# Kernel optimization log

Measured on AMD Instinct MI355X. Metric: run time of the kernel, lower is better.

Reference implementation:

```python
import jax, jax.numpy as jnp
import numpy as np

D = 768
LAYERS = 4
LN_EPS = 1e-5


def _layer_norm(h, g, b):
    m = jnp.mean(h, axis=-1, keepdims=True)
    v = jnp.var(h, axis=-1, keepdims=True)
    return (h - m) * jax.lax.rsqrt(v + LN_EPS) * g + b


def _encode(ids, emb, ln_g, ln_b, w1, b1, w2, b2):
    # ids: [N, F] int, emb: [F, V, D] stacked embedding tables
    h = emb[0][ids[:, 0]]
    for i in range(1, emb.shape[0]):
        h = h + emb[i][ids[:, i]]
    h = _layer_norm(h, ln_g, ln_b)
    h = jax.nn.gelu(jnp.dot(h, w1) + b1)
    return jnp.dot(h, w2) + b2


def setup_inputs() -> dict:
    key = jax.random.key(0)
    ks = jax.random.split(key, 24)
    N, E = 50000, 100000
    s = 0.02
    inp = {
        "x": jax.random.randint(ks[0], (N, 9), 0, 128),
        "edge_attr": jax.random.randint(ks[1], (E, 3), 0, 8),
        "edge_index": jax.random.randint(ks[2], (2, E), 0, N),
        # AtomEncoder params
        "atom_emb": jax.random.normal(ks[3], (9, 128, D), jnp.float32) * s,
        "atom_ln_g": jnp.ones((D,), jnp.float32),
        "atom_ln_b": jnp.zeros((D,), jnp.float32),
        "atom_w1": jax.random.normal(ks[4], (D, D), jnp.float32) * s,
        "atom_b1": jnp.zeros((D,), jnp.float32),
        "atom_w2": jax.random.normal(ks[5], (D, D), jnp.float32) * s,
        "atom_b2": jnp.zeros((D,), jnp.float32),
        # BondEncoder params
        "bond_emb": jax.random.normal(ks[6], (3, 8, D), jnp.float32) * s,
        "bond_ln_g": jnp.ones((D,), jnp.float32),
        "bond_ln_b": jnp.zeros((D,), jnp.float32),
        "bond_w1": jax.random.normal(ks[7], (D, D), jnp.float32) * s,
        "bond_b1": jnp.zeros((D,), jnp.float32),
        "bond_w2": jax.random.normal(ks[8], (D, D), jnp.float32) * s,
        "bond_b2": jnp.zeros((D,), jnp.float32),
        # Per-layer GINEConv MLPs + LayerNorms (stacked over layers)
        "conv_w1": jax.random.normal(ks[9], (LAYERS, D, D), jnp.float32) * s,
        "conv_b1": jnp.zeros((LAYERS, D), jnp.float32),
        "conv_w2": jax.random.normal(ks[10], (LAYERS, D, D), jnp.float32) * s,
        "conv_b2": jnp.zeros((LAYERS, D), jnp.float32),
        "ln_g": jnp.ones((LAYERS, D), jnp.float32),
        "ln_b": jnp.zeros((LAYERS, D), jnp.float32),
    }
    return inp


def reference(x, edge_attr, edge_index,
              atom_emb, atom_ln_g, atom_ln_b, atom_w1, atom_b1, atom_w2, atom_b2,
              bond_emb, bond_ln_g, bond_ln_b, bond_w1, bond_b1, bond_w2, bond_b2,
              conv_w1, conv_b1, conv_w2, conv_b2, ln_g, ln_b):
    N = x.shape[0]
    src, dst = edge_index[0], edge_index[1]
    h = _encode(x, atom_emb, atom_ln_g, atom_ln_b, atom_w1, atom_b1, atom_w2, atom_b2)
    e = _encode(edge_attr, bond_emb, bond_ln_g, bond_ln_b, bond_w1, bond_b1, bond_w2, bond_b2)
    for l in range(LAYERS):
        h_in = h
        # GINEConv (eps=0): out = MLP(x + sum_{j in N(i)} relu(x_j + e_ij))
        msg = jax.nn.relu(h[src] + e)                       # [E, D] gather + edge-add + relu
        agg = jax.ops.segment_sum(msg, dst, num_segments=N)  # scatter-add to nodes
        z = h + agg
        z = jnp.dot(jax.nn.relu(jnp.dot(z, conv_w1[l]) + conv_b1[l]), conv_w2[l]) + conv_b2[l]
        # gelu -> dropout (identity at eval) -> residual LayerNorm
        h = _layer_norm(jax.nn.gelu(z) + h_in, ln_g[l], ln_b[l])
    return h
```

## Files before the change

### kernel.cpp

```cpp
#include <hip/hip_runtime.h>


#define DM 768
#define NLAYERS 4
#define CHUNK 50048

typedef _Float16 f16;
typedef __attribute__((ext_vector_type(8))) _Float16 f16x8;
typedef __attribute__((ext_vector_type(4))) _Float16 f16x4;
typedef __attribute__((ext_vector_type(4))) float f32x4;

__device__ __forceinline__ float gelu_f(float x) {
    float u = 0.7978845608028654f * (x + 0.044715f * x * x * x);
    float a = __expf(-2.0f * fabsf(u));
    float t = (1.0f - a) / (1.0f + a);
    t = copysignf(t, u);
    return 0.5f * x * (1.0f + t);
}
__device__ __forceinline__ void async16(const void* g, void* l) {
    __builtin_amdgcn_global_load_lds((const __attribute__((address_space(1))) void*)g,
                                     (__attribute__((address_space(3))) void*)l,
                                     16, 0, 0);
}

__device__ __forceinline__ int xcd_swizzle(int b, int nb) {
    int xcd = b & 7;
    int pos = b >> 3;
    int q = nb >> 3, r = nb & 7;
    int base = (xcd < r) ? xcd * (q + 1) : r * (q + 1) + (xcd - r) * q;
    return base + pos;
}

__global__ __launch_bounds__(256) void transpose768(
    const float* __restrict__ W, f16* __restrict__ Wt) {
    __shared__ float t[32][33];
    int tx = threadIdx.x, ty = threadIdx.y;
    int c0 = blockIdx.x * 32, r0 = blockIdx.y * 32;
    #pragma unroll
    for (int j = 0; j < 32; j += 8) t[ty + j][tx] = W[(r0 + ty + j) * DM + c0 + tx];
    __syncthreads();
    #pragma unroll
    for (int j = 0; j < 32; j += 8) Wt[(long)(c0 + ty + j) * DM + r0 + tx] = (f16)t[tx][ty + j];
}

__global__ __launch_bounds__(256) void embed_ln_wave(
    const int* __restrict__ ids, int F, int V,
    const float* __restrict__ emb,
    const float* __restrict__ g, const float* __restrict__ b,
    f16* __restrict__ out, int M) {
    int row = blockIdx.x * 4 + (threadIdx.x >> 6);
    if (row >= M) return;
    int lane = threadIdx.x & 63;
    int base = lane * 12;

    float v[12];
    #pragma unroll
    for (int j = 0; j < 12; ++j) v[j] = 0.f;
    for (int f = 0; f < F; ++f) {
        int id = ids[(long)row * F + f];
        const float* r = emb + ((long)f * V + id) * DM + base;
        float4 r0 = *(const float4*)&r[0];
        float4 r1 = *(const float4*)&r[4];
        float4 r2 = *(const float4*)&r[8];
        v[0] += r0.x; v[1] += r0.y; v[2]  += r0.z; v[3]  += r0.w;
        v[4] += r1.x; v[5] += r1.y; v[6]  += r1.z; v[7]  += r1.w;
        v[8] += r2.x; v[9] += r2.y; v[10] += r2.z; v[11] += r2.w;
    }
    float s1 = 0.f, s2 = 0.f;
    #pragma unroll
    for (int j = 0; j < 12; ++j) { s1 += v[j]; s2 += v[j] * v[j]; }
    #pragma unroll
    for (int off = 32; off > 0; off >>= 1) {
        s1 += __shfl_xor(s1, off);
        s2 += __shfl_xor(s2, off);
    }
    float mean = s1 * (1.f / DM);
    float var = s2 * (1.f / DM) - mean * mean;
    float rstd = rsqrtf(var + 1e-5f);

    float4 gv0 = *(const float4*)&g[base], gv1 = *(const float4*)&g[base + 4], gv2 = *(const float4*)&g[base + 8];
    float4 bv0 = *(const float4*)&b[base], bv1 = *(const float4*)&b[base + 4], bv2 = *(const float4*)&b[base + 8];
    float gg[12] = {gv0.x, gv0.y, gv0.z, gv0.w, gv1.x, gv1.y, gv1.z, gv1.w, gv2.x, gv2.y, gv2.z, gv2.w};
    float bb[12] = {bv0.x, bv0.y, bv0.z, bv0.w, bv1.x, bv1.y, bv1.z, bv1.w, bv2.x, bv2.y, bv2.z, bv2.w};
    f16* o = out + (long)row * DM + base;
    #pragma unroll
    for (int q = 0; q < 3; ++q) {
        f16x4 ov;
        #pragma unroll
        for (int r = 0; r < 4; ++r)
            ov[r] = (f16)((v[q * 4 + r] - mean) * rstd * gg[q * 4 + r] + bb[q * 4 + r]);
        *(f16x4*)&o[q * 4] = ov;
    }
}

template <typename OUT>
__global__ __launch_bounds__(256) void gelu_res_ln_wave(
    const f16* __restrict__ U, const f16* __restrict__ hin,
    const float* __restrict__ g, const float* __restrict__ b,
    OUT* __restrict__ out, int M) {
    int row = blockIdx.x * 4 + (threadIdx.x >> 6);
    if (row >= M) return;
    int lane = threadIdx.x & 63;
    int base = lane * 12;

    const f16* up = U + (long)row * DM + base;
    const f16* hp = hin + (long)row * DM + base;
    float v[12];
    #pragma unroll
    for (int q = 0; q < 3; ++q) {
        f16x4 uv = *(const f16x4*)&up[q * 4];
        f16x4 hv = *(const f16x4*)&hp[q * 4];
        #pragma unroll
        for (int r = 0; r < 4; ++r)
            v[q * 4 + r] = gelu_f((float)uv[r]) + (float)hv[r];
    }
    float s1 = 0.f, s2 = 0.f;
    #pragma unroll
    for (int j = 0; j < 12; ++j) { s1 += v[j]; s2 += v[j] * v[j]; }
    #pragma unroll
    for (int off = 32; off > 0; off >>= 1) {
        s1 += __shfl_xor(s1, off);
        s2 += __shfl_xor(s2, off);
    }
    float mean = s1 * (1.f / DM);
    float var = s2 * (1.f / DM) - mean * mean;
    float rstd = rsqrtf(var + 1e-5f);

    float4 gv0 = *(const float4*)&g[base], gv1 = *(const float4*)&g[base + 4], gv2 = *(const float4*)&g[base + 8];
    float4 bv0 = *(const float4*)&b[base], bv1 = *(const float4*)&b[base + 4], bv2 = *(const float4*)&b[base + 8];
    float gg[12] = {gv0.x, gv0.y, gv0.z, gv0.w, gv1.x, gv1.y, gv1.z, gv1.w, gv2.x, gv2.y, gv2.z, gv2.w};
    float bb[12] = {bv0.x, bv0.y, bv0.z, bv0.w, bv1.x, bv1.y, bv1.z, bv1.w, bv2.x, bv2.y, bv2.z, bv2.w};
    #pragma unroll
    for (int q = 0; q < 3; ++q) {
        float w0 = (v[q * 4 + 0] - mean) * rstd * gg[q * 4 + 0] + bb[q * 4 + 0];
        float w1 = (v[q * 4 + 1] - mean) * rstd * gg[q * 4 + 1] + bb[q * 4 + 1];
        float w2 = (v[q * 4 + 2] - mean) * rstd * gg[q * 4 + 2] + bb[q * 4 + 2];
        float w3 = (v[q * 4 + 3] - mean) * rstd * gg[q * 4 + 3] + bb[q * 4 + 3];
        if constexpr (sizeof(OUT) == 2) {
            f16x4 ov; ov[0] = (f16)w0; ov[1] = (f16)w1; ov[2] = (f16)w2; ov[3] = (f16)w3;
            *(f16x4*)&out[(long)row * DM + base + q * 4] = ov;
        } else {
            float4 ov; ov.x = w0; ov.y = w1; ov.z = w2; ov.w = w3;
            *(float4*)&out[(long)row * DM + base + q * 4] = ov;
        }
    }
}

__global__ __launch_bounds__(256) void make_combo_ids(
    int V, int nC, int* __restrict__ ids) {
    int c = blockIdx.x * 256 + threadIdx.x;
    if (c >= nC) return;
    ids[c * 3 + 0] = c / (V * V);
    ids[c * 3 + 1] = (c / V) % V;
    ids[c * 3 + 2] = c % V;
}
__global__ __launch_bounds__(256) void make_key_kernel(
    const int* __restrict__ ea, int E, int V, int* __restrict__ key) {
    int e = blockIdx.x * 256 + threadIdx.x;
    if (e >= E) return;
    key[e] = (ea[e * 3 + 0] * V + ea[e * 3 + 1]) * V + ea[e * 3 + 2];
}

__global__ __launch_bounds__(256) void build_list_kernel(
    const int* __restrict__ ei, int E,
    int* __restrict__ head, int* __restrict__ nxt) {
    int e = blockIdx.x * 256 + threadIdx.x;
    if (e >= E) return;
    int dst = ei[E + e];
    nxt[e] = atomicExch(&head[dst], e);
}

__global__ __launch_bounds__(256) void gather_agg_kernel(
    const int* __restrict__ ei,
    const int* __restrict__ head, const int* __restrict__ nxt,
    const int* __restrict__ key,
    const f16* __restrict__ h, const f16* __restrict__ T,
    f16* __restrict__ z, int N) {
    int node = blockIdx.x * 4 + (threadIdx.x >> 6);
    if (node >= N) return;
    int lane = threadIdx.x & 63;
    int base = lane * 12;

    const f16* hr = h + (long)node * DM + base;
    f16x4 v0 = *(const f16x4*)&hr[0];
    f16x4 v1 = *(const f16x4*)&hr[4];
    f16x4 v2 = *(const f16x4*)&hr[8];
    float acc[12];
    #pragma unroll
    for (int j = 0; j < 4; ++j) {
        acc[j]     = (float)v0[j];
        acc[4 + j] = (float)v1[j];
        acc[8 + j] = (float)v2[j];
    }

    int ecur = head[node];
    while (ecur >= 0) {
        int enext = nxt[ecur];
        int src = ei[ecur];
        int kq = key[ecur];
        const f16* sr = h + (long)src * DM + base;
        const f16* er = T + (long)kq * DM + base;
        f16x4 a0 = *(const f16x4*)&sr[0];
        f16x4 a1 = *(const f16x4*)&sr[4];
        f16x4 a2 = *(const f16x4*)&sr[8];
        f16x4 b0 = *(const f16x4*)&er[0];
        f16x4 b1 = *(const f16x4*)&er[4];
        f16x4 b2 = *(const f16x4*)&er[8];
        #pragma unroll
        for (int j = 0; j < 4; ++j) {
            float m0 = (float)a0[j] + (float)b0[j];
            float m1 = (float)a1[j] + (float)b1[j];
            float m2 = (float)a2[j] + (float)b2[j];
            if (m0 > 0.f) acc[j]     += m0;
            if (m1 > 0.f) acc[4 + j] += m1;
            if (m2 > 0.f) acc[8 + j] += m2;
        }
        ecur = enext;
    }

    f16* zr = z + (long)node * DM + base;
    f16x4 o0, o1, o2;
    #pragma unroll
    for (int j = 0; j < 4; ++j) {
        o0[j] = (f16)acc[j];
        o1[j] = (f16)acc[4 + j];
        o2[j] = (f16)acc[8 + j];
    }
    *(f16x4*)&zr[0] = o0;
    *(f16x4*)&zr[4] = o1;
    *(f16x4*)&zr[8] = o2;
}

#define ACT_NONE 0
#define ACT_RELU 1
#define ACT_GELU 2

template <int ACT>
__global__ __launch_bounds__(256, 2) void gemm768(
    const f16* __restrict__ A,
    const f16* __restrict__ Bt,
    const float* __restrict__ bias,
    f16* __restrict__ C,
    int M) {
    __shared__ f16 As[128 * 64];
    __shared__ f16 Bs[128 * 64];
    int tid = threadIdx.x;
    int lane = tid & 63;
    int wid = tid >> 6;
    int wm = wid >> 1, wn = wid & 1;

    int wg = xcd_swizzle(blockIdx.x, gridDim.x);
    int rt = wg / 6, cb = wg - rt * 6;
    long rowBase = (long)rt * 128;
    const f16* Ab = A + rowBase * DM;
    const f16* Bb = Bt + (long)cb * 128 * DM;

    f32x4 acc[4][4];
    #pragma unroll
    for (int i = 0; i < 4; ++i)
        #pragma unroll
        for (int j = 0; j < 4; ++j) acc[i][j] = (f32x4){0.f, 0.f, 0.f, 0.f};

    int sr = wid * 32;
    int srow = lane >> 3;
    int sslot = lane & 7;
    int scol = ((sslot ^ srow) * 8);
    const f16* gA = Ab + (long)(sr + srow) * DM + scol;
    const f16* gB = Bb + (long)(sr + srow) * DM + scol;

    int fm = lane & 15;
    int fq = lane >> 4;
    int rs0 = ((fq ^ (fm & 7)) * 8);
    int rs1 = (((4 + fq) ^ (fm & 7)) * 8);

    for (int kt = 0; kt < DM / 64; ++kt) {
        int k0 = kt * 64;
        #pragma unroll
        for (int j = 0; j < 4; ++j) {
            async16(gA + k0 + j * 8 * DM, &As[(sr + j * 8) * 64]);
            async16(gB + k0 + j * 8 * DM, &Bs[(sr + j * 8) * 64]);
        }
        __syncthreads();

        f16x8 af0[4], bf0[4], af1[4], bf1[4];
        #pragma unroll
        for (int i = 0; i < 4; ++i) {
            int ra = (wm * 64 + i * 16 + fm) * 64;
            af0[i] = *(const f16x8*)&As[ra + rs0];
            af1[i] = *(const f16x8*)&As[ra + rs1];
        }
        #pragma unroll
        for (int j = 0; j < 4; ++j) {
            int rb = (wn * 64 + j * 16 + fm) * 64;
            bf0[j] = *(const f16x8*)&Bs[rb + rs0];
            bf1[j] = *(const f16x8*)&Bs[rb + rs1];
        }
        #pragma unroll
        for (int ci = 0; ci < 4; ++ci)
            #pragma unroll
            for (int ri = 0; ri < 4; ++ri)
                acc[ci][ri] = __builtin_amdgcn_mfma_f32_16x16x32_f16(bf0[ci], af0[ri], acc[ci][ri], 0, 0, 0);
        #pragma unroll
        for (int ci = 0; ci < 4; ++ci)
            #pragma unroll
            for (int ri = 0; ri < 4; ++ri)
                acc[ci][ri] = __builtin_amdgcn_mfma_f32_16x16x32_f16(bf1[ci], af1[ri], acc[ci][ri], 0, 0, 0);
        __syncthreads();
    }

    int row0 = (int)rowBase + wm * 64;
    int col0 = cb * 128 + wn * 64;
    float4 bv[4];
    #pragma unroll
    for (int ci = 0; ci < 4; ++ci)
        bv[ci] = *(const float4*)&bias[col0 + ci * 16 + (lane >> 4) * 4];
    #pragma unroll
    for (int ri = 0; ri < 4; ++ri) {
        int row = row0 + ri * 16 + (lane & 15);
        if (row < M) {
            #pragma unroll
            for (int ci = 0; ci < 4; ++ci) {
                int c0 = col0 + ci * 16 + (lane >> 4) * 4;
                f16x4 o;
                #pragma unroll
                for (int r = 0; r < 4; ++r) {
                    float v = acc[ci][ri][r] + (&bv[ci].x)[r];
                    if (ACT == ACT_RELU) v = v > 0.f ? v : 0.f;
                    if (ACT == ACT_GELU) v = gelu_f(v);
                    o[r] = (f16)v;
                }
                *(f16x4*)&C[(long)row * DM + c0] = o;
            }
        }
    }
}

extern "C" void kernel_launch(void* const* d_in, const int* in_sizes, int n_in,
                              void* d_out, int out_size, void* d_ws, size_t ws_size,
                              hipStream_t stream) {
    const int* x  = (const int*)d_in[0];
    const int* ea = (const int*)d_in[1];
    const int* ei = (const int*)d_in[2];
    const float* atom_emb  = (const float*)d_in[3];
    const float* atom_ln_g = (const float*)d_in[4];
    const float* atom_ln_b = (const float*)d_in[5];
    const float* atom_w1   = (const float*)d_in[6];
    const float* atom_b1   = (const float*)d_in[7];
    const float* atom_w2   = (const float*)d_in[8];
    const float* atom_b2   = (const float*)d_in[9];
    const float* bond_emb  = (const float*)d_in[10];
    const float* bond_ln_g = (const float*)d_in[11];
    const float* bond_ln_b = (const float*)d_in[12];
    const float* bond_w1   = (const float*)d_in[13];
    const float* bond_b1   = (const float*)d_in[14];
    const float* bond_w2   = (const float*)d_in[15];
    const float* bond_b2   = (const float*)d_in[16];
    const float* conv_w1   = (const float*)d_in[17];
    const float* conv_b1   = (const float*)d_in[18];
    const float* conv_w2   = (const float*)d_in[19];
    const float* conv_b2   = (const float*)d_in[20];
    const float* ln_g      = (const float*)d_in[21];
    const float* ln_b      = (const float*)d_in[22];

    const int N = in_sizes[0] / 9;
    const int E = in_sizes[1] / 3;
    const int V = in_sizes[10] / (3 * DM);
    const int nC = V * V * V;
    const long SZ = (long)DM * DM;

    char* ws = (char*)d_ws;
    size_t off = 0;
    f16* WT  = (f16*)(ws + off); off += ((size_t)12 * SZ * 2 + 4095) & ~(size_t)4095;
    f16* Q   = (f16*)(ws + off); off += ((size_t)CHUNK * DM * 2 + 4095) & ~(size_t)4095;
    f16* h   = (f16*)(ws + off); off += ((size_t)N * DM * 2 + 4095) & ~(size_t)4095;
    f16* T   = (f16*)(ws + off); off += ((size_t)((nC + 127) & ~127) * DM * 2 + 4095) & ~(size_t)4095;
    int* key = (int*)(ws + off); off += ((size_t)E * 4 + 4095) & ~(size_t)4095;
    int* ids3 = (int*)(ws + off); off += ((size_t)nC * 12 + 4095) & ~(size_t)4095;
    f16*   U    = (f16*)d_out;
    int*   head = (int*)((char*)d_out + 120000000);
    int*   nxt  = head + N;

    dim3 tb(32, 8), tg(24, 24);
    transpose768<<<tg, tb, 0, stream>>>(atom_w1, WT + 0 * SZ);
    transpose768<<<tg, tb, 0, stream>>>(atom_w2, WT + 1 * SZ);
    transpose768<<<tg, tb, 0, stream>>>(bond_w1, WT + 2 * SZ);
    transpose768<<<tg, tb, 0, stream>>>(bond_w2, WT + 3 * SZ);
    for (int l = 0; l < NLAYERS; ++l) {
        transpose768<<<tg, tb, 0, stream>>>(conv_w1 + l * SZ, WT + (4 + l) * SZ);
        transpose768<<<tg, tb, 0, stream>>>(conv_w2 + l * SZ, WT + (8 + l) * SZ);
    }

    hipMemsetAsync(head, 0xFF, (size_t)N * 4, stream);
    build_list_kernel<<<(E + 255) / 256, 256, 0, stream>>>(ei, E, head, nxt);
    make_key_kernel<<<(E + 255) / 256, 256, 0, stream>>>(ea, E, V, key);

    int rtN = (N + 127) / 128;
    dim3 gn(6 * rtN);

    embed_ln_wave<<<(N + 3) / 4, 256, 0, stream>>>(x, 9, 128, atom_emb, atom_ln_g, atom_ln_b, Q, N);
    gemm768<ACT_GELU><<<gn, 256, 0, stream>>>(Q, WT + 0 * SZ, atom_b1, U, N);
    gemm768<ACT_NONE><<<gn, 256, 0, stream>>>(U, WT + 1 * SZ, atom_b2, h, N);

    make_combo_ids<<<(nC + 255) / 256, 256, 0, stream>>>(V, nC, ids3);
    embed_ln_wave<<<(nC + 3) / 4, 256, 0, stream>>>(ids3, 3, V, bond_emb, bond_ln_g, bond_ln_b, Q, nC);
    dim3 gt(6 * ((nC + 127) / 128));
    gemm768<ACT_GELU><<<gt, 256, 0, stream>>>(Q, WT + 2 * SZ, bond_b1, U, nC);
    gemm768<ACT_NONE><<<gt, 256, 0, stream>>>(U, WT + 3 * SZ, bond_b2, T, nC);

    for (int l = 0; l < NLAYERS; ++l) {
        gather_agg_kernel<<<(N + 3) / 4, 256, 0, stream>>>(ei, head, nxt, key, h, T, Q, N);
        gemm768<ACT_RELU><<<gn, 256, 0, stream>>>(Q, WT + (4 + l) * SZ, conv_b1 + l * DM, U, N);
        gemm768<ACT_NONE><<<gn, 256, 0, stream>>>(U, WT + (8 + l) * SZ, conv_b2 + l * DM, Q, N);
        if (l == NLAYERS - 1) {
            gelu_res_ln_wave<float><<<(N + 3) / 4, 256, 0, stream>>>(Q, h, ln_g + l * DM, ln_b + l * DM, (float*)d_out, N);
        } else {
            gelu_res_ln_wave<f16><<<(N + 3) / 4, 256, 0, stream>>>(Q, h, ln_g + l * DM, ln_b + l * DM, h, N);
        }
    }
}
```

Measured before the change: 1.377 ms.

## Replace 128x128 GEMM with double-buffered 256x256 tile, 512-thread pipelined kernel

The 768-wide GEMM moves from a 128x128 tile with 256 threads and a single LDS buffer to a 256x256 tile with 512 threads (8 waves) and double-buffered LDS. The next K-tile's async loads are interleaved with the MFMA phases, gated by explicit vmcnt waits and barriers, and setprio raises wave priority during the MFMA blocks. The aim is to hide global-memory latency and raise operand reuse per LDS byte. In exchange it uses 128KB of LDS and more accumulator registers per wave, which limits occupancy. The larger tiles also add padding waste on M and give fewer blocks for the bond-combination GEMM.

```diff
diff --git a/kernel.cpp b/kernel.cpp
--- a/kernel.cpp
+++ b/kernel.cpp
@@ -235,96 +235,102 @@
 #define ACT_RELU 1
 #define ACT_GELU 2
 
+#define STAGE_PAIR(i, ktile, buf)                                                            \
+    async16(gA + (long)(ktile) * 64 + (long)(i) * 64 * DM, &As[buf][((i) * 64 + wid * 8) * 64]); \
+    async16(gB + (long)(ktile) * 64 + (long)(i) * 64 * DM, &Bs[buf][((i) * 64 + wid * 8) * 64]);
+
 template <int ACT>
-__global__ __launch_bounds__(256, 2) void gemm768(
+__global__ __launch_bounds__(512, 2) void gemm256(
     const f16* __restrict__ A,
     const f16* __restrict__ Bt,
     const float* __restrict__ bias,
     f16* __restrict__ C,
     int M) {
-    __shared__ f16 As[128 * 64];
-    __shared__ f16 Bs[128 * 64];
+    __shared__ f16 As[2][256 * 64];
+    __shared__ f16 Bs[2][256 * 64];
     int tid = threadIdx.x;
     int lane = tid & 63;
     int wid = tid >> 6;
-    int wm = wid >> 1, wn = wid & 1;
+    int wm = wid >> 2, wn = wid & 3;
 
     int wg = xcd_swizzle(blockIdx.x, gridDim.x);
-    int rt = wg / 6, cb = wg - rt * 6;
-    long rowBase = (long)rt * 128;
+    int rt = wg / 3, cb = wg - rt * 3;
+    long rowBase = (long)rt * 256;
     const f16* Ab = A + rowBase * DM;
-    const f16* Bb = Bt + (long)cb * 128 * DM;
-
-    f32x4 acc[4][4];
-    #pragma unroll
-    for (int i = 0; i < 4; ++i)
+    const f16* Bb = Bt + (long)cb * 256 * DM;
+
+    int srow8 = lane >> 3;
+    int sslot = lane & 7;
+    int scol = ((sslot ^ srow8) * 8);
+    const f16* gA = Ab + (long)(wid * 8 + srow8) * DM + scol;
+    const f16* gB = Bb + (long)(wid * 8 + srow8) * DM + scol;
+
+    int fm = lane & 15;
+    int fq = lane >> 4;
+
+    int col0 = cb * 256 + wn * 64;
+    float4 bv[4];
+    #pragma unroll
+    for (int ci = 0; ci < 4; ++ci)
+        bv[ci] = *(const float4*)&bias[col0 + ci * 16 + fq * 4];
+
+    f32x4 acc[8][4];
+    #pragma unroll
+    for (int i = 0; i < 8; ++i)
         #pragma unroll
         for (int j = 0; j < 4; ++j) acc[i][j] = (f32x4){0.f, 0.f, 0.f, 0.f};
 
-    int sr = wid * 32;
-    int srow = lane >> 3;
-    int sslot = lane & 7;
-    int scol = ((sslot ^ srow) * 8);
-    const f16* gA = Ab + (long)(sr + srow) * DM + scol;
-    const f16* gB = Bb + (long)(sr + srow) * DM + scol;
-
-    int fm = lane & 15;
-    int fq = lane >> 4;
-    int rs0 = ((fq ^ (fm & 7)) * 8);
-    int rs1 = (((4 + fq) ^ (fm & 7)) * 8);
-
+    #pragma unroll
+    for (int i = 0; i < 4; ++i) { STAGE_PAIR(i, 0, 0) }
+
+    int cur = 0;
     for (int kt = 0; kt < DM / 64; ++kt) {
-        int k0 = kt * 64;
+        int nxtb = cur ^ 1;
+        bool pre = (kt + 1 < DM / 64);
+        __builtin_amdgcn_sched_barrier(0);
+        if (pre) { STAGE_PAIR(0, kt + 1, nxtb) }
+        if (pre) asm volatile("s_waitcnt vmcnt(2)" ::: "memory");
+        else     asm volatile("s_waitcnt vmcnt(0)" ::: "memory");
+        __builtin_amdgcn_s_barrier();
+        __builtin_amdgcn_sched_barrier(0);
+
         #pragma unroll
-        for (int j = 0; j < 4; ++j) {
-            async16(gA + k0 + j * 8 * DM, &As[(sr + j * 8) * 64]);
-            async16(gB + k0 + j * 8 * DM, &Bs[(sr + j * 8) * 64]);
+        for (int p = 0; p < 4; ++p) {
+            const int rih = p & 1, kh = p >> 1;
+            int rs = ((kh * 4 + fq) ^ (fm & 7)) * 8;
+            f16x8 af[4], bf[4];
+            #pragma unroll
+            for (int r = 0; r < 4; ++r)
+                af[r] = *(const f16x8*)&As[cur][(wm * 128 + (rih * 4 + r) * 16 + fm) * 64 + rs];
+            #pragma unroll
+            for (int c = 0; c < 4; ++c)
+                bf[c] = *(const f16x8*)&Bs[cur][(wn * 64 + c * 16 + fm) * 64 + rs];
+            if (pre && p > 0) { STAGE_PAIR(p, kt + 1, nxtb) }
+            __builtin_amdgcn_s_setprio(1);
+            #pragma unroll
+            for (int c = 0; c < 4; ++c)
+                #pragma unroll
+                for (int r = 0; r < 4; ++r)
+                    acc[rih * 4 + r][c] = __builtin_amdgcn_mfma_f32_16x16x32_f16(
+                        bf[c], af[r], acc[rih * 4 + r][c], 0, 0, 0);
+            __builtin_amdgcn_s_setprio(0);
+            __builtin_amdgcn_s_barrier();
         }
-        __syncthreads();
-
-        f16x8 af0[4], bf0[4], af1[4], bf1[4];
-        #pragma unroll
-        for (int i = 0; i < 4; ++i) {
-            int ra = (wm * 64 + i * 16 + fm) * 64;
-            af0[i] = *(const f16x8*)&As[ra + rs0];
-            af1[i] = *(const f16x8*)&As[ra + rs1];
-        }
-        #pragma unroll
-        for (int j = 0; j < 4; ++j) {
-            int rb = (wn * 64 + j * 16 + fm) * 64;
-            bf0[j] = *(const f16x8*)&Bs[rb + rs0];
-            bf1[j] = *(const f16x8*)&Bs[rb + rs1];
-        }
-        #pragma unroll
-        for (int ci = 0; ci < 4; ++ci)
-            #pragma unroll
-            for (int ri = 0; ri < 4; ++ri)
-                acc[ci][ri] = __builtin_amdgcn_mfma_f32_16x16x32_f16(bf0[ci], af0[ri], acc[ci][ri], 0, 0, 0);
-        #pragma unroll
-        for (int ci = 0; ci < 4; ++ci)
-            #pragma unroll
-            for (int ri = 0; ri < 4; ++ri)
-                acc[ci][ri] = __builtin_amdgcn_mfma_f32_16x16x32_f16(bf1[ci], af1[ri], acc[ci][ri], 0, 0, 0);
-        __syncthreads();
-    }
-
-    int row0 = (int)rowBase + wm * 64;
-    int col0 = cb * 128 + wn * 64;
-    float4 bv[4];
-    #pragma unroll
-    for (int ci = 0; ci < 4; ++ci)
-        bv[ci] = *(const float4*)&bias[col0 + ci * 16 + (lane >> 4) * 4];
-    #pragma unroll
-    for (int ri = 0; ri < 4; ++ri) {
-        int row = row0 + ri * 16 + (lane & 15);
+        cur = nxtb;
+    }
+
+    int row0 = (int)rowBase + wm * 128;
+    #pragma unroll
+    for (int ri = 0; ri < 8; ++ri) {
+        int row = row0 + ri * 16 + fm;
         if (row < M) {
             #pragma unroll
             for (int ci = 0; ci < 4; ++ci) {
-                int c0 = col0 + ci * 16 + (lane >> 4) * 4;
+                int c0 = col0 + ci * 16 + fq * 4;
                 f16x4 o;
                 #pragma unroll
                 for (int r = 0; r < 4; ++r) {
-                    float v = acc[ci][ri][r] + (&bv[ci].x)[r];
+                    float v = acc[ri][ci][r] + (&bv[ci].x)[r];
                     if (ACT == ACT_RELU) v = v > 0.f ? v : 0.f;
                     if (ACT == ACT_GELU) v = gelu_f(v);
                     o[r] = (f16)v;
@@ -373,7 +379,7 @@
     f16* WT  = (f16*)(ws + off); off += ((size_t)12 * SZ * 2 + 4095) & ~(size_t)4095;
     f16* Q   = (f16*)(ws + off); off += ((size_t)CHUNK * DM * 2 + 4095) & ~(size_t)4095;
     f16* h   = (f16*)(ws + off); off += ((size_t)N * DM * 2 + 4095) & ~(size_t)4095;
-    f16* T   = (f16*)(ws + off); off += ((size_t)((nC + 127) & ~127) * DM * 2 + 4095) & ~(size_t)4095;
+    f16* T   = (f16*)(ws + off); off += ((size_t)((nC + 255) & ~255) * DM * 2 + 4095) & ~(size_t)4095;
     int* key = (int*)(ws + off); off += ((size_t)E * 4 + 4095) & ~(size_t)4095;
     int* ids3 = (int*)(ws + off); off += ((size_t)nC * 12 + 4095) & ~(size_t)4095;
     f16*   U    = (f16*)d_out;
@@ -394,23 +400,22 @@
     build_list_kernel<<<(E + 255) / 256, 256, 0, stream>>>(ei, E, head, nxt);
     make_key_kernel<<<(E + 255) / 256, 256, 0, stream>>>(ea, E, V, key);
 
-    int rtN = (N + 127) / 128;
-    dim3 gn(6 * rtN);
+    dim3 gn(3 * ((N + 255) / 256));
 
     embed_ln_wave<<<(N + 3) / 4, 256, 0, stream>>>(x, 9, 128, atom_emb, atom_ln_g, atom_ln_b, Q, N);
-    gemm768<ACT_GELU><<<gn, 256, 0, stream>>>(Q, WT + 0 * SZ, atom_b1, U, N);
-    gemm768<ACT_NONE><<<gn, 256, 0, stream>>>(U, WT + 1 * SZ, atom_b2, h, N);
+    gemm256<ACT_GELU><<<gn, 512, 0, stream>>>(Q, WT + 0 * SZ, atom_b1, U, N);
+    gemm256<ACT_NONE><<<gn, 512, 0, stream>>>(U, WT + 1 * SZ, atom_b2, h, N);
 
     make_combo_ids<<<(nC + 255) / 256, 256, 0, stream>>>(V, nC, ids3);
     embed_ln_wave<<<(nC + 3) / 4, 256, 0, stream>>>(ids3, 3, V, bond_emb, bond_ln_g, bond_ln_b, Q, nC);
-    dim3 gt(6 * ((nC + 127) / 128));
-    gemm768<ACT_GELU><<<gt, 256, 0, stream>>>(Q, WT + 2 * SZ, bond_b1, U, nC);
-    gemm768<ACT_NONE><<<gt, 256, 0, stream>>>(U, WT + 3 * SZ, bond_b2, T, nC);
+    dim3 gt(3 * ((nC + 255) / 256));
+    gemm256<ACT_GELU><<<gt, 512, 0, stream>>>(Q, WT + 2 * SZ, bond_b1, U, nC);
+    gemm256<ACT_NONE><<<gt, 512, 0, stream>>>(U, WT + 3 * SZ, bond_b2, T, nC);
 
     for (int l = 0; l < NLAYERS; ++l) {
         gather_agg_kernel<<<(N + 3) / 4, 256, 0, stream>>>(ei, head, nxt, key, h, T, Q, N);
-        gemm768<ACT_RELU><<<gn, 256, 0, stream>>>(Q, WT + (4 + l) * SZ, conv_b1 + l * DM, U, N);
-        gemm768<ACT_NONE><<<gn, 256, 0, stream>>>(U, WT + (8 + l) * SZ, conv_b2 + l * DM, Q, N);
+        gemm256<ACT_RELU><<<gn, 512, 0, stream>>>(Q, WT + (4 + l) * SZ, conv_b1 + l * DM, U, N);
+        gemm256<ACT_NONE><<<gn, 512, 0, stream>>>(U, WT + (8 + l) * SZ, conv_b2 + l * DM, Q, N);
         if (l == NLAYERS - 1) {
             gelu_res_ln_wave<float><<<(N + 3) / 4, 256, 0, stream>>>(Q, h, ln_g + l * DM, ln_b + l * DM, (float*)d_out, N);
         } else {
```

New measurement: 1.669 ms. 21.2% more time.
